# Kernel optimization log

Measured on AMD Instinct MI355X. Metric: run time of the kernel, lower is better.

## Reference

```python
import jax, jax.numpy as jnp
import numpy as np

B, D_IN, HID, LAT, K = 8192, 1024, 2048, 256, 4096

def setup_inputs() -> dict:
    key = jax.random.key(0)
    ks = jax.random.split(key, 16)
    s = lambda fan_in: 1.0 / np.sqrt(fan_in)
    inp = {
        'x':  jax.random.normal(ks[0], (B, D_IN), jnp.float32),
        # encoder MLP
        'W1': jax.random.normal(ks[1], (D_IN, HID), jnp.float32) * s(D_IN),
        'b1': jnp.zeros((HID,), jnp.float32),
        'W2': jax.random.normal(ks[2], (HID, HID), jnp.float32) * s(HID),
        'b2': jnp.zeros((HID,), jnp.float32),
        'W3': jax.random.normal(ks[3], (HID, LAT), jnp.float32) * s(HID),
        'b3': jnp.zeros((LAT,), jnp.float32),
        # codebook, uniform(-1/K, 1/K) per nn.init.uniform_
        'embed': jax.random.uniform(ks[4], (K, LAT), jnp.float32, -1.0 / K, 1.0 / K),
        # decoder MLP
        'D1': jax.random.normal(ks[5], (LAT, HID), jnp.float32) * s(LAT),
        'd1': jnp.zeros((HID,), jnp.float32),
        'D2': jax.random.normal(ks[6], (HID, HID), jnp.float32) * s(HID),
        'd2': jnp.zeros((HID,), jnp.float32),
        'D3': jax.random.normal(ks[7], (HID, D_IN), jnp.float32) * s(HID),
        'd3': jnp.zeros((D_IN,), jnp.float32),
    }
    return inp

def gelu(x):
    return jax.nn.gelu(x, approximate=False)  # torch nn.GELU default is exact erf

def reference(x, W1, b1, W2, b2, W3, b3, embed, D1, d1, D2, d2, D3, d3):
    sg = jax.lax.stop_gradient
    # encoder: [B, D_in] -> [B, latent]
    h = gelu(x @ W1 + b1)
    h = gelu(h @ W2 + b2)
    z_e = h @ W3 + b3
    # squared distances to codebook: ||z||^2 + ||e||^2 - 2 z.e -> [B, K]
    z_sq = jnp.sum(z_e * z_e, axis=1, keepdims=True)
    e_sq = jnp.sum(embed * embed, axis=1)[None, :]
    dist = z_sq + e_sq - 2.0 * (z_e @ embed.T)
    indices = jnp.argmin(dist, axis=1)            # [B]
    z_q = embed[indices]                          # [B, latent]
    commitment = jnp.mean((z_e - sg(z_q)) ** 2)
    codebook = jnp.mean((z_q - sg(z_e)) ** 2)
    vq_loss = codebook + 0.25 * commitment
    # straight-through estimator
    z_st = z_e + sg(z_q - z_e)
    # decoder: [B, latent] -> [B, D_in]
    g = gelu(z_st @ D1 + d1)
    g = gelu(g @ D2 + d2)
    x_recon = g @ D3 + d3
    return x_recon, vq_loss, indices
```

## Files before the change

kernel.cpp:

```cpp
#include <hip/hip_runtime.h>
#include <math.h>

#define B_    8192
#define DIN_  1024
#define HID_  2048
#define LAT_  256
#define KC_   4096

using bfrag8 = __attribute__((ext_vector_type(8))) short;
using short8 = __attribute__((ext_vector_type(8))) short;
using half8  = __attribute__((ext_vector_type(8))) _Float16;
using facc4  = __attribute__((ext_vector_type(4))) float;

__device__ __forceinline__ unsigned short f2bf(float f) {
    union { float f; unsigned int u; } c; c.f = f;
    unsigned int u = c.u;
    return (unsigned short)((u + 0x7FFFu + ((u >> 16) & 1u)) >> 16);
}

__device__ __forceinline__ unsigned short f2h_bits(float f) {
    union { _Float16 h; unsigned short u; } c; c.h = (_Float16)f;
    return c.u;
}

__device__ __forceinline__ void gload16(const unsigned short* g, unsigned short* l) {
    __builtin_amdgcn_global_load_lds(
        (const __attribute__((address_space(1))) void*)(g),
        (__attribute__((address_space(3))) void*)(l), 16, 0, 0);
}

template <int GELU, int OUT_SPLIT>
__global__ __launch_bounds__(512, 4) void gemm_split_f16_w8(
    const unsigned short* __restrict__ Ahi, const unsigned short* __restrict__ Alo,
    const unsigned short* __restrict__ WThi, const unsigned short* __restrict__ WTlo,
    const float* __restrict__ bias,
    unsigned short* __restrict__ Chi, unsigned short* __restrict__ Clo,
    float* __restrict__ Cf32,
    int M, int N, int K)
{
    __shared__ __align__(16) unsigned short AsH[128 * 64];
    __shared__ __align__(16) unsigned short AsL[128 * 64];
    __shared__ __align__(16) unsigned short WsH[128 * 64];
    __shared__ __align__(16) unsigned short WsL[128 * 64];

    const int tid  = threadIdx.x;
    const int wave = tid >> 6;
    const int lane = tid & 63;
    const int wm   = wave & 1;
    const int wn   = wave >> 1;
    const int quad = lane >> 4;
    const int ln   = lane & 15;
    const int n0 = blockIdx.x * 128;
    const int m0 = blockIdx.y * 128;

    const facc4 fz4 = {0.0f, 0.0f, 0.0f, 0.0f};
    facc4 accA[4][2] = {};
    facc4 accB[4][2] = {};
    facc4 master[4][2] = {};

    for (int k0 = 0; k0 < K; k0 += 64) {
#pragma unroll
        for (int i = 0; i < 2; ++i) {
            const int idx = i * 512 + tid;
            const int row = idx >> 3;
            const int gs  = (idx & 7) ^ (row & 7);
            const int wb  = i * 512 + (tid & 448);
            const size_t src = (size_t)(m0 + row) * K + k0 + gs * 8;
            gload16(&Ahi[src], &AsH[wb * 8]);
            gload16(&Alo[src], &AsL[wb * 8]);
        }
#pragma unroll
        for (int i = 0; i < 2; ++i) {
            const int idx = i * 512 + tid;
            const int row = idx >> 3;
            const int gs  = (idx & 7) ^ (row & 7);
            const int wb  = i * 512 + (tid & 448);
            const size_t src = (size_t)(n0 + row) * K + k0 + gs * 8;
            gload16(&WThi[src], &WsH[wb * 8]);
            gload16(&WTlo[src], &WsL[wb * 8]);
        }
        __syncthreads();
#pragma unroll
        for (int ks = 0; ks < 64; ks += 32) {
            const int gq = (ks >> 3) + quad;
            half8 aH[4], aL[4], bH[2], bL[2];
#pragma unroll
            for (int f = 0; f < 4; ++f) {
                const int row = wm * 64 + f * 16 + ln;
                const int off = row * 64 + ((gq ^ (ln & 7)) << 3);
                aH[f] = *reinterpret_cast<const half8*>(&AsH[off]);
                aL[f] = *reinterpret_cast<const half8*>(&AsL[off]);
            }
#pragma unroll
            for (int f = 0; f < 2; ++f) {
                const int row = wn * 32 + f * 16 + ln;
                const int off = row * 64 + ((gq ^ (ln & 7)) << 3);
                bH[f] = *reinterpret_cast<const half8*>(&WsH[off]);
                bL[f] = *reinterpret_cast<const half8*>(&WsL[off]);
            }
#pragma unroll
            for (int fm = 0; fm < 4; ++fm)
#pragma unroll
                for (int fn = 0; fn < 2; ++fn)
                    accA[fm][fn] = __builtin_amdgcn_mfma_f32_16x16x32_f16(
                        aH[fm], bH[fn], accA[fm][fn], 0, 0, 0);
#pragma unroll
            for (int fm = 0; fm < 4; ++fm)
#pragma unroll
                for (int fn = 0; fn < 2; ++fn)
                    accB[fm][fn] = __builtin_amdgcn_mfma_f32_16x16x32_f16(
                        aH[fm], bL[fn], accB[fm][fn], 0, 0, 0);
#pragma unroll
            for (int fm = 0; fm < 4; ++fm)
#pragma unroll
                for (int fn = 0; fn < 2; ++fn)
                    accB[fm][fn] = __builtin_amdgcn_mfma_f32_16x16x32_f16(
                        aL[fm], bH[fn], accB[fm][fn], 0, 0, 0);
        }
        __syncthreads();
        if ((k0 & 192) == 192) {
#pragma unroll
            for (int fm = 0; fm < 4; ++fm)
#pragma unroll
                for (int fn = 0; fn < 2; ++fn) {
                    master[fm][fn] += accA[fm][fn];
                    accA[fm][fn] = fz4;
                }
        }
    }

    const double SC_HI = 0.015625;
    const double SC_LO = 3.814697265625e-06;
#pragma unroll
    for (int fn = 0; fn < 2; ++fn) {
        const int col = n0 + wn * 32 + fn * 16 + ln;
        const double bb = (double)bias[col];
#pragma unroll
        for (int fm = 0; fm < 4; ++fm) {
            const int rbase = m0 + wm * 64 + fm * 16 + quad * 4;
#pragma unroll
            for (int r = 0; r < 4; ++r) {
                double v = (double)master[fm][fn][r] * SC_HI
                         + (double)accB[fm][fn][r] * SC_LO + bb;
                if (GELU) v = 0.5 * v * (1.0 + erf(v * 0.70710678118654752440));
                const float hf = (float)v;
                if (OUT_SPLIT == 1 || OUT_SPLIT == 2) {
                    const _Float16 hi = (_Float16)hf;
                    const float lo = (hf - (float)hi) * 4096.0f;
                    union { _Float16 h; unsigned short u; } c1, c2;
                    c1.h = hi; c2.h = (_Float16)lo;
                    Chi[(size_t)(rbase + r) * N + col] = c1.u;
                    Clo[(size_t)(rbase + r) * N + col] = c2.u;
                }
                if (OUT_SPLIT == 0 || OUT_SPLIT == 2) {
                    Cf32[(size_t)(rbase + r) * N + col] = hf;
                }
            }
        }
    }
}

template <int GELU, int OUT_SPLIT>
__global__ __launch_bounds__(256, 3) void gemm_split_f16(
    const unsigned short* __restrict__ Ahi, const unsigned short* __restrict__ Alo,
    const unsigned short* __restrict__ WThi, const unsigned short* __restrict__ WTlo,
    const float* __restrict__ bias,
    unsigned short* __restrict__ Chi, unsigned short* __restrict__ Clo,
    float* __restrict__ Cf32,
    int M, int N, int K)
{
    __shared__ __align__(16) unsigned short AsH[128 * 64];
    __shared__ __align__(16) unsigned short AsL[128 * 64];
    __shared__ __align__(16) unsigned short WsH[64 * 64];
    __shared__ __align__(16) unsigned short WsL[64 * 64];

    const int tid  = threadIdx.x;
    const int wave = tid >> 6;
    const int lane = tid & 63;
    const int wm   = wave & 1;
    const int wn   = wave >> 1;
    const int quad = lane >> 4;
    const int ln   = lane & 15;
    const int n0 = blockIdx.x * 64;
    const int m0 = blockIdx.y * 128;

    const facc4 fz4 = {0.0f, 0.0f, 0.0f, 0.0f};
    facc4 accA[4][2] = {};
    facc4 accB[4][2] = {};
    facc4 master[4][2] = {};

    for (int k0 = 0; k0 < K; k0 += 64) {
#pragma unroll
        for (int i = 0; i < 4; ++i) {
            const int idx = i * 256 + tid;
            const int row = idx >> 3;
            const int gs  = (idx & 7) ^ (row & 7);
            const int wb  = i * 256 + (tid & 192);
            const size_t src = (size_t)(m0 + row) * K + k0 + gs * 8;
            gload16(&Ahi[src], &AsH[wb * 8]);
            gload16(&Alo[src], &AsL[wb * 8]);
        }
#pragma unroll
        for (int i = 0; i < 2; ++i) {
            const int idx = i * 256 + tid;
            const int row = idx >> 3;
            const int gs  = (idx & 7) ^ (row & 7);
            const int wb  = i * 256 + (tid & 192);
            const size_t src = (size_t)(n0 + row) * K + k0 + gs * 8;
            gload16(&WThi[src], &WsH[wb * 8]);
            gload16(&WTlo[src], &WsL[wb * 8]);
        }
        __syncthreads();
#pragma unroll
        for (int ks = 0; ks < 64; ks += 32) {
            const int gq = (ks >> 3) + quad;
            half8 aH[4], aL[4], bH[2], bL[2];
#pragma unroll
            for (int f = 0; f < 4; ++f) {
                const int row = wm * 64 + f * 16 + ln;
                const int off = row * 64 + ((gq ^ (ln & 7)) << 3);
                aH[f] = *reinterpret_cast<const half8*>(&AsH[off]);
                aL[f] = *reinterpret_cast<const half8*>(&AsL[off]);
            }
#pragma unroll
            for (int f = 0; f < 2; ++f) {
                const int row = wn * 32 + f * 16 + ln;
                const int off = row * 64 + ((gq ^ (ln & 7)) << 3);
                bH[f] = *reinterpret_cast<const half8*>(&WsH[off]);
                bL[f] = *reinterpret_cast<const half8*>(&WsL[off]);
            }
#pragma unroll
            for (int fm = 0; fm < 4; ++fm)
#pragma unroll
                for (int fn = 0; fn < 2; ++fn)
                    accA[fm][fn] = __builtin_amdgcn_mfma_f32_16x16x32_f16(
                        aH[fm], bH[fn], accA[fm][fn], 0, 0, 0);
#pragma unroll
            for (int fm = 0; fm < 4; ++fm)
#pragma unroll
                for (int fn = 0; fn < 2; ++fn)
                    accB[fm][fn] = __builtin_amdgcn_mfma_f32_16x16x32_f16(
                        aH[fm], bL[fn], accB[fm][fn], 0, 0, 0);
#pragma unroll
            for (int fm = 0; fm < 4; ++fm)
#pragma unroll
                for (int fn = 0; fn < 2; ++fn)
                    accB[fm][fn] = __builtin_amdgcn_mfma_f32_16x16x32_f16(
                        aL[fm], bH[fn], accB[fm][fn], 0, 0, 0);
        }
        __syncthreads();
        if ((k0 & 192) == 192) {
#pragma unroll
            for (int fm = 0; fm < 4; ++fm)
#pragma unroll
                for (int fn = 0; fn < 2; ++fn) {
                    master[fm][fn] += accA[fm][fn];
                    accA[fm][fn] = fz4;
                }
        }
    }

    const double SC_HI = 0.015625;
    const double SC_LO = 3.814697265625e-06;
#pragma unroll
    for (int fn = 0; fn < 2; ++fn) {
        const int col = n0 + wn * 32 + fn * 16 + ln;
        const double bb = (double)bias[col];
#pragma unroll
        for (int fm = 0; fm < 4; ++fm) {
            const int rbase = m0 + wm * 64 + fm * 16 + quad * 4;
#pragma unroll
            for (int r = 0; r < 4; ++r) {
                double v = (double)master[fm][fn][r] * SC_HI
                         + (double)accB[fm][fn][r] * SC_LO + bb;
                if (GELU) v = 0.5 * v * (1.0 + erf(v * 0.70710678118654752440));
                const float hf = (float)v;
                if (OUT_SPLIT == 1 || OUT_SPLIT == 2) {
                    const _Float16 hi = (_Float16)hf;
                    const float lo = (hf - (float)hi) * 4096.0f;
                    union { _Float16 h; unsigned short u; } c1, c2;
                    c1.h = hi; c2.h = (_Float16)lo;
                    Chi[(size_t)(rbase + r) * N + col] = c1.u;
                    Clo[(size_t)(rbase + r) * N + col] = c2.u;
                }
                if (OUT_SPLIT == 0 || OUT_SPLIT == 2) {
                    Cf32[(size_t)(rbase + r) * N + col] = hf;
                }
            }
        }
    }
}

__global__ __launch_bounds__(256) void split_scaled_f16x2(
    const float* __restrict__ X, unsigned short* __restrict__ Xhi,
    unsigned short* __restrict__ Xlo, int n4, float scale)
{
    const int i = blockIdx.x * 256 + threadIdx.x;
    if (i >= n4) return;
    const float4 v = reinterpret_cast<const float4*>(X)[i];
    ushort4 h, l;
    {
        const float s = v.x * scale;
        _Float16 a = (_Float16)s; h.x = f2h_bits((float)a); l.x = f2h_bits((s - (float)a) * 4096.0f);
    }
    {
        const float s = v.y * scale;
        _Float16 a = (_Float16)s; h.y = f2h_bits((float)a); l.y = f2h_bits((s - (float)a) * 4096.0f);
    }
    {
        const float s = v.z * scale;
        _Float16 a = (_Float16)s; h.z = f2h_bits((float)a); l.z = f2h_bits((s - (float)a) * 4096.0f);
    }
    {
        const float s = v.w * scale;
        _Float16 a = (_Float16)s; h.w = f2h_bits((float)a); l.w = f2h_bits((s - (float)a) * 4096.0f);
    }
    reinterpret_cast<ushort4*>(Xhi)[i] = h;
    reinterpret_cast<ushort4*>(Xlo)[i] = l;
}

__global__ __launch_bounds__(64) void emb_prep(
    const float* __restrict__ E, float* __restrict__ esq,
    unsigned short* __restrict__ Ehi, unsigned short* __restrict__ Elo,
    float* __restrict__ loss_slot)
{
    const int r = blockIdx.x;
    const float4 v = reinterpret_cast<const float4*>(E + (size_t)r * LAT_)[threadIdx.x];
    ushort4 h, l;
    {
        const float s = v.x * 65536.0f;
        _Float16 a = (_Float16)s; h.x = f2h_bits((float)a); l.x = f2h_bits((s - (float)a) * 4096.0f);
    }
    {
        const float s = v.y * 65536.0f;
        _Float16 a = (_Float16)s; h.y = f2h_bits((float)a); l.y = f2h_bits((s - (float)a) * 4096.0f);
    }
    {
        const float s = v.z * 65536.0f;
        _Float16 a = (_Float16)s; h.z = f2h_bits((float)a); l.z = f2h_bits((s - (float)a) * 4096.0f);
    }
    {
        const float s = v.w * 65536.0f;
        _Float16 a = (_Float16)s; h.w = f2h_bits((float)a); l.w = f2h_bits((s - (float)a) * 4096.0f);
    }
    reinterpret_cast<ushort4*>(Ehi + (size_t)r * LAT_)[threadIdx.x] = h;
    reinterpret_cast<ushort4*>(Elo + (size_t)r * LAT_)[threadIdx.x] = l;
    double s = (double)v.x * v.x + (double)v.y * v.y + (double)v.z * v.z + (double)v.w * v.w;
#pragma unroll
    for (int off = 32; off; off >>= 1) s += __shfl_down(s, off, 64);
    if (threadIdx.x == 0) {
        esq[r] = (float)s;
        if (r == 0) *loss_slot = 0.0f;
    }
}

__global__ __launch_bounds__(256) void wsplit_transpose(
    const float* __restrict__ W, unsigned short* __restrict__ WThi,
    unsigned short* __restrict__ WTlo, int K, int N)
{
    __shared__ float t[32][33];
    const int k0 = blockIdx.x * 32;
    const int n0 = blockIdx.y * 32;
    const int x = threadIdx.x;
    const int y = threadIdx.y;
#pragma unroll
    for (int i = 0; i < 4; ++i)
        t[y + i * 8][x] = W[(size_t)(k0 + y + i * 8) * N + n0 + x];
    __syncthreads();
#pragma unroll
    for (int i = 0; i < 4; ++i) {
        const float w = t[x][y + i * 8] * 64.0f;
        const _Float16 hi = (_Float16)w;
        const float lo = (w - (float)hi) * 4096.0f;
        WThi[(size_t)(n0 + y + i * 8) * K + k0 + x] = f2h_bits((float)hi);
        WTlo[(size_t)(n0 + y + i * 8) * K + k0 + x] = f2h_bits(lo);
    }
}

__global__ __launch_bounds__(256, 2) void vq_argmin_mfma(
    const unsigned short* __restrict__ Zhi, const unsigned short* __restrict__ Zlo,
    const unsigned short* __restrict__ Ehi, const unsigned short* __restrict__ Elo,
    const float* __restrict__ esq, const float* __restrict__ zsq,
    float* __restrict__ pval, int* __restrict__ pidx)
{
    __shared__ __align__(16) unsigned short ZsH[128 * 64];
    __shared__ __align__(16) unsigned short ZsL[128 * 64];
    __shared__ __align__(16) unsigned short EsH[64 * 64];
    __shared__ __align__(16) unsigned short EsL[64 * 64];
    __shared__ float rbv[128][2];
    __shared__ int   rbi[128][2];

    const int tid  = threadIdx.x;
    const int wave = tid >> 6;
    const int lane = tid & 63;
    const int wm   = wave & 1;
    const int wn   = wave >> 1;
    const int quad = lane >> 4;
    const int ln   = lane & 15;
    const int m0    = blockIdx.x * 128;
    const int split = blockIdx.y;

    float zsqv[4][4];
#pragma unroll
    for (int fm = 0; fm < 4; ++fm) {
        const float4 q = *reinterpret_cast<const float4*>(
            &zsq[m0 + wm * 64 + fm * 16 + quad * 4]);
        zsqv[fm][0] = q.x; zsqv[fm][1] = q.y; zsqv[fm][2] = q.z; zsqv[fm][3] = q.w;
    }

    float bestv[4][4];
    int   besti[4][4];
#pragma unroll
    for (int a = 0; a < 4; ++a)
#pragma unroll
        for (int b = 0; b < 4; ++b) { bestv[a][b] = 3.4e38f; besti[a][b] = 0; }

    for (int nt = 0; nt < 8; ++nt) {
        const int n0 = split * 512 + nt * 64;
        facc4 accA[4][2] = {};
        facc4 accB[4][2] = {};
        for (int k0 = 0; k0 < 256; k0 += 64) {
            __syncthreads();
#pragma unroll
            for (int i = 0; i < 4; ++i) {
                const int idx = i * 256 + tid;
                const int row = idx >> 3;
                const int gs  = (idx & 7) ^ (row & 7);
                const int wb  = i * 256 + (tid & 192);
                const size_t src = (size_t)(m0 + row) * LAT_ + k0 + gs * 8;
                gload16(&Zhi[src], &ZsH[wb * 8]);
                gload16(&Zlo[src], &ZsL[wb * 8]);
            }
#pragma unroll
            for (int i = 0; i < 2; ++i) {
                const int idx = i * 256 + tid;
                const int row = idx >> 3;
                const int gs  = (idx & 7) ^ (row & 7);
                const int wb  = i * 256 + (tid & 192);
                const size_t src = (size_t)(n0 + row) * LAT_ + k0 + gs * 8;
                gload16(&Ehi[src], &EsH[wb * 8]);
                gload16(&Elo[src], &EsL[wb * 8]);
            }
            __syncthreads();
#pragma unroll
            for (int ks = 0; ks < 64; ks += 32) {
                const int gq = (ks >> 3) + quad;
                half8 aH[4], aL[4], bH[2], bL[2];
#pragma unroll
                for (int f = 0; f < 4; ++f) {
                    const int row = wm * 64 + f * 16 + ln;
                    const int off = row * 64 + ((gq ^ (ln & 7)) << 3);
                    aH[f] = *reinterpret_cast<const half8*>(&ZsH[off]);
                    aL[f] = *reinterpret_cast<const half8*>(&ZsL[off]);
                }
#pragma unroll
                for (int f = 0; f < 2; ++f) {
                    const int row = wn * 32 + f * 16 + ln;
                    const int off = row * 64 + ((gq ^ (ln & 7)) << 3);
                    bH[f] = *reinterpret_cast<const half8*>(&EsH[off]);
                    bL[f] = *reinterpret_cast<const half8*>(&EsL[off]);
                }
#pragma unroll
                for (int fm = 0; fm < 4; ++fm)
#pragma unroll
                    for (int fn = 0; fn < 2; ++fn)
                        accA[fm][fn] = __builtin_amdgcn_mfma_f32_16x16x32_f16(
                            aH[fm], bH[fn], accA[fm][fn], 0, 0, 0);
#pragma unroll
                for (int fm = 0; fm < 4; ++fm)
#pragma unroll
                    for (int fn = 0; fn < 2; ++fn)
                        accB[fm][fn] = __builtin_amdgcn_mfma_f32_16x16x32_f16(
                            aH[fm], bL[fn], accB[fm][fn], 0, 0, 0);
#pragma unroll
                for (int fm = 0; fm < 4; ++fm)
#pragma unroll
                    for (int fn = 0; fn < 2; ++fn)
                        accB[fm][fn] = __builtin_amdgcn_mfma_f32_16x16x32_f16(
                            aL[fm], bH[fn], accB[fm][fn], 0, 0, 0);
            }
        }
#pragma unroll
        for (int fm = 0; fm < 4; ++fm)
#pragma unroll
            for (int fn = 0; fn < 2; ++fn) {
                const int n = n0 + wn * 32 + fn * 16 + ln;
                const float es = esq[n];
#pragma unroll
                for (int r = 0; r < 4; ++r) {
                    const float pa = accA[fm][fn][r] * 0x1p-15f;
                    const float pb = accB[fm][fn][r] * 0x1p-27f;
                    const float t2m = pa + pb;
                    const float sc = (zsqv[fm][r] + es) - t2m;
                    if (sc < bestv[fm][r]) { bestv[fm][r] = sc; besti[fm][r] = n; }
                }
            }
    }

#pragma unroll
    for (int fm = 0; fm < 4; ++fm)
#pragma unroll
        for (int r = 0; r < 4; ++r) {
            float v0 = bestv[fm][r]; int i0 = besti[fm][r];
#pragma unroll
            for (int mask = 1; mask < 16; mask <<= 1) {
                const float v2 = __shfl_xor(v0, mask, 64);
                const int   i2 = __shfl_xor(i0, mask, 64);
                if (v2 < v0 || (v2 == v0 && i2 < i0)) { v0 = v2; i0 = i2; }
            }
            bestv[fm][r] = v0; besti[fm][r] = i0;
        }

    if (ln == 0) {
#pragma unroll
        for (int fm = 0; fm < 4; ++fm)
#pragma unroll
            for (int r = 0; r < 4; ++r) {
                const int rl = wm * 64 + fm * 16 + quad * 4 + r;
                rbv[rl][wn] = bestv[fm][r];
                rbi[rl][wn] = besti[fm][r];
            }
    }
    __syncthreads();
    if (tid < 128) {
        float bv = rbv[tid][0]; int bi = rbi[tid][0];
        const float v = rbv[tid][1]; const int ix = rbi[tid][1];
        if (v < bv || (v == bv && ix < bi)) { bv = v; bi = ix; }
        pval[(size_t)(m0 + tid) * 8 + split] = bv;
        pidx[(m0 + tid) * 8 + split] = bi;
    }
}

template <int OUT_BF16>
__global__ __launch_bounds__(256) void gemm_mfma_bf16(
    const unsigned short* __restrict__ A,
    const unsigned short* __restrict__ WT,
    const float* __restrict__ bias,
    void* __restrict__ Cout,
    int M, int N, int K)
{
    __shared__ __align__(16) unsigned short As[128 * 64];
    __shared__ __align__(16) unsigned short Bs[128 * 64];

    const int tid  = threadIdx.x;
    const int wave = tid >> 6;
    const int lane = tid & 63;
    const int wm   = wave & 1;
    const int wn   = wave >> 1;
    const int quad = lane >> 4;
    const int ln   = lane & 15;
    const int m0 = blockIdx.x * 128;
    const int n0 = blockIdx.y * 128;

    facc4 acc[4][4] = {};

    for (int k0 = 0; k0 < K; k0 += 64) {
#pragma unroll
        for (int i = 0; i < 4; ++i) {
            const int idx = i * 256 + tid;
            const int row = idx >> 3;
            const int c8  = (idx & 7) * 8;
            const int wb  = i * 256 + (tid & 192);
            gload16(&A[(size_t)(m0 + row) * K + k0 + c8], &As[wb * 8]);
            gload16(&WT[(size_t)(n0 + row) * K + k0 + c8], &Bs[wb * 8]);
        }
        __syncthreads();
#pragma unroll
        for (int ks = 0; ks < 64; ks += 32) {
            bfrag8 am[4], bn[4];
#pragma unroll
            for (int f = 0; f < 4; ++f) {
                am[f] = *reinterpret_cast<const bfrag8*>(
                    &As[(wm * 64 + f * 16 + ln) * 64 + ks + quad * 8]);
                bn[f] = *reinterpret_cast<const bfrag8*>(
                    &Bs[(wn * 64 + f * 16 + ln) * 64 + ks + quad * 8]);
            }
#pragma unroll
            for (int fm = 0; fm < 4; ++fm)
#pragma unroll
                for (int fn = 0; fn < 4; ++fn)
                    acc[fm][fn] = __builtin_amdgcn_mfma_f32_16x16x32_bf16(
                        am[fm], bn[fn], acc[fm][fn], 0, 0, 0);
        }
        __syncthreads();
    }

#pragma unroll
    for (int fn = 0; fn < 4; ++fn) {
        const int col = n0 + wn * 64 + fn * 16 + ln;
        const float bf = bias[col];
#pragma unroll
        for (int fm = 0; fm < 4; ++fm) {
            const int rbase = m0 + wm * 64 + fm * 16 + quad * 4;
#pragma unroll
            for (int r = 0; r < 4; ++r) {
                float v = acc[fm][fn][r] + bf;
                if (OUT_BF16) {
                    v = 0.5f * v * (1.0f + erff(v * 0.70710678118654752440f));
                    ((unsigned short*)Cout)[(size_t)(rbase + r) * N + col] = f2bf(v);
                } else {
                    ((float*)Cout)[(size_t)(rbase + r) * N + col] = v;
                }
            }
        }
    }
}

__global__ __launch_bounds__(256) void cast_transpose_w3(
    const float* __restrict__ D1w, unsigned short* __restrict__ wt1,
    const float* __restrict__ D2w, unsigned short* __restrict__ wt2,
    const float* __restrict__ D3w, unsigned short* __restrict__ wt3)
{
    const int bid = blockIdx.x;
    const float* W; unsigned short* WT; int K, N, kt, nt;
    if (bid < 512)        { W = D1w; WT = wt1; K = LAT_; N = HID_; kt = bid & 7;  nt = bid >> 3; }
    else if (bid < 4608)  { const int l = bid - 512;  W = D2w; WT = wt2; K = HID_; N = HID_; kt = l & 63; nt = l >> 6; }
    else                  { const int l = bid - 4608; W = D3w; WT = wt3; K = HID_; N = DIN_; kt = l & 63; nt = l >> 6; }

    __shared__ float t[32][33];
    const int k0 = kt * 32;
    const int n0 = nt * 32;
    const int x = threadIdx.x;
    const int y = threadIdx.y;
#pragma unroll
    for (int i = 0; i < 4; ++i)
        t[y + i * 8][x] = W[(size_t)(k0 + y + i * 8) * N + n0 + x];
    __syncthreads();
#pragma unroll
    for (int i = 0; i < 4; ++i)
        WT[(size_t)(n0 + y + i * 8) * K + k0 + x] = f2bf(t[x][y + i * 8]);
}

__global__ __launch_bounds__(64) void rowsq_kernel(
    const float* __restrict__ X, float* __restrict__ out,
    float* __restrict__ loss_slot)
{
    const int r = blockIdx.x;
    const float4 v = reinterpret_cast<const float4*>(X + (size_t)r * LAT_)[threadIdx.x];
    double s = (double)v.x * v.x + (double)v.y * v.y + (double)v.z * v.z + (double)v.w * v.w;
#pragma unroll
    for (int off = 32; off; off >>= 1) s += __shfl_down(s, off, 64);
    if (threadIdx.x == 0) {
        out[r] = (float)s;
        if (loss_slot != nullptr && r == 0) *loss_slot = 0.0f;
    }
}

__global__ __launch_bounds__(64) void vq_finalize(
    const float* __restrict__ pval, const int* __restrict__ pidx,
    const float* __restrict__ Z, const float* __restrict__ E,
    unsigned short* __restrict__ zqb, float* __restrict__ out_idx,
    float* __restrict__ loss_slot)
{
    const int row = blockIdx.x;
    __shared__ int sidx;
    if (threadIdx.x == 0) {
        float bv = pval[row * 8]; int bi = pidx[row * 8];
#pragma unroll
        for (int s = 1; s < 8; ++s) {
            const float v = pval[row * 8 + s]; const int ix = pidx[row * 8 + s];
            if (v < bv || (v == bv && ix < bi)) { bv = v; bi = ix; }
        }
        sidx = bi;
        out_idx[row] = (float)bi;
    }
    __syncthreads();
    const int idx = sidx;
    const float4 e = reinterpret_cast<const float4*>(E + (size_t)idx * LAT_)[threadIdx.x];
    const float4 z = reinterpret_cast<const float4*>(Z + (size_t)row * LAT_)[threadIdx.x];
    ushort4 q; q.x = f2bf(e.x); q.y = f2bf(e.y); q.z = f2bf(e.z); q.w = f2bf(e.w);
    reinterpret_cast<ushort4*>(zqb + (size_t)row * LAT_)[threadIdx.x] = q;
    const float dx = z.x - e.x, dy = z.y - e.y, dz = z.z - e.z, dw = z.w - e.w;
    float s = dx * dx + dy * dy + dz * dz + dw * dw;
#pragma unroll
    for (int off = 32; off; off >>= 1) s += __shfl_down(s, off, 64);
    if (threadIdx.x == 0)
        atomicAdd(loss_slot, s * (1.25f / ((float)B_ * (float)LAT_)));
}

extern "C" void kernel_launch(void* const* d_in, const int* in_sizes, int n_in,
                              void* d_out, int out_size, void* d_ws, size_t ws_size,
                              hipStream_t stream)
{
    const float* x   = (const float*)d_in[0];
    const float* W1  = (const float*)d_in[1];
    const float* b1  = (const float*)d_in[2];
    const float* W2  = (const float*)d_in[3];
    const float* b2  = (const float*)d_in[4];
    const float* W3  = (const float*)d_in[5];
    const float* b3  = (const float*)d_in[6];
    const float* emb = (const float*)d_in[7];
    const float* D1  = (const float*)d_in[8];
    const float* d1  = (const float*)d_in[9];
    const float* D2  = (const float*)d_in[10];
    const float* d2  = (const float*)d_in[11];
    const float* D3  = (const float*)d_in[12];
    const float* d3  = (const float*)d_in[13];
    float* out = (float*)d_out;

    char* ws = (char*)d_ws;
    const size_t MB = 1u << 20;
    unsigned short* h1hi = (unsigned short*)(ws);
    unsigned short* h1lo = (unsigned short*)(ws + 32 * MB);
    unsigned short* zehi = (unsigned short*)(ws);
    unsigned short* zelo = (unsigned short*)(ws + 4 * MB);
    unsigned short* g1b  = (unsigned short*)(ws);
    unsigned short* zqb  = (unsigned short*)(ws + 32 * MB);
    unsigned short* g2b  = (unsigned short*)(ws + 32 * MB);
    unsigned short* xhi  = (unsigned short*)(ws + 64 * MB);
    unsigned short* xlo  = (unsigned short*)(ws + 80 * MB);
    unsigned short* h2hi = (unsigned short*)(ws + 64 * MB);
    unsigned short* h2lo = (unsigned short*)(ws + 96 * MB);
    unsigned short* wt1  = (unsigned short*)(ws + 64 * MB);
    unsigned short* wt2  = (unsigned short*)(ws + 65 * MB);
    unsigned short* wt3  = (unsigned short*)(ws + 73 * MB);
    float* ze = (float*)(ws + 128 * MB);
    unsigned short* w1thi = (unsigned short*)(ws + 136 * MB);
    unsigned short* w1tlo = (unsigned short*)(ws + 140 * MB);
    unsigned short* w2thi = (unsigned short*)(ws + 136 * MB);
    unsigned short* w2tlo = (unsigned short*)(ws + 144 * MB);
    unsigned short* w3thi = (unsigned short*)(ws + 136 * MB);
    unsigned short* w3tlo = (unsigned short*)(ws + 137 * MB);
    unsigned short* ehi   = (unsigned short*)(ws + 144 * MB);
    unsigned short* elo   = (unsigned short*)(ws + 146 * MB);
    float* esq  = (float*)(ws + 152 * MB);
    float* zsq  = (float*)(ws + 152 * MB + 64 * 1024);
    float* pval = (float*)(ws + 152 * MB + 128 * 1024);
    int*   pidx = (int*)  (ws + 152 * MB + 384 * 1024);

    float* loss_slot = out + (size_t)B_ * DIN_;
    float* out_idx   = loss_slot + 1;

    split_scaled_f16x2<<<(B_ * DIN_ / 4 + 255) / 256, 256, 0, stream>>>(
        x, xhi, xlo, B_ * DIN_ / 4, 1.0f);
    wsplit_transpose<<<dim3(DIN_ / 32, HID_ / 32), dim3(32, 8), 0, stream>>>(W1, w1thi, w1tlo, DIN_, HID_);

    gemm_split_f16_w8<1, 1><<<dim3(HID_ / 128, B_ / 128), 512, 0, stream>>>(
        xhi, xlo, w1thi, w1tlo, b1, h1hi, h1lo, nullptr, B_, HID_, DIN_);

    wsplit_transpose<<<dim3(HID_ / 32, HID_ / 32), dim3(32, 8), 0, stream>>>(W2, w2thi, w2tlo, HID_, HID_);

    gemm_split_f16_w8<1, 1><<<dim3(HID_ / 128, B_ / 128), 512, 0, stream>>>(
        h1hi, h1lo, w2thi, w2tlo, b2, h2hi, h2lo, nullptr, B_, HID_, HID_);

    emb_prep<<<KC_, 64, 0, stream>>>(emb, esq, ehi, elo, loss_slot);
    wsplit_transpose<<<dim3(HID_ / 32, LAT_ / 32), dim3(32, 8), 0, stream>>>(W3, w3thi, w3tlo, HID_, LAT_);

    gemm_split_f16<0, 2><<<dim3(LAT_ / 64, B_ / 128), 256, 0, stream>>>(
        h2hi, h2lo, w3thi, w3tlo, b3, zehi, zelo, ze, B_, LAT_, HID_);

    rowsq_kernel<<<B_, 64, 0, stream>>>(ze, zsq, nullptr);

    cast_transpose_w3<<<6656, dim3(32, 8), 0, stream>>>(D1, wt1, D2, wt2, D3, wt3);

    vq_argmin_mfma<<<dim3(B_ / 128, 8), 256, 0, stream>>>(
        zehi, zelo, ehi, elo, esq, zsq, pval, pidx);
    vq_finalize<<<B_, 64, 0, stream>>>(pval, pidx, ze, emb, zqb, out_idx, loss_slot);

    gemm_mfma_bf16<1><<<dim3(B_ / 128, HID_ / 128), 256, 0, stream>>>(zqb, wt1, d1, (void*)g1b, B_, HID_, LAT_);
    gemm_mfma_bf16<1><<<dim3(B_ / 128, HID_ / 128), 256, 0, stream>>>(g1b, wt2, d2, (void*)g2b, B_, HID_, HID_);
    gemm_mfma_bf16<0><<<dim3(B_ / 128, DIN_ / 128), 256, 0, stream>>>(g2b, wt3, d3, (void*)out, B_, DIN_, HID_);
}
```

Baseline: 1.134 ms.

## Fuse prep kernels into two launches and retile split-f16 GEMMs

Merges the x split, W1/W2/W3 split-transposes into one prep_all launch, and the embedding prep plus decoder weight cast-transposes into one mid_prep launch, rearranging workspace so the buffers don't alias. The encoder GEMMs drop the 512-thread 128x128 tile for the 256-thread 128x64 kernel, and the W3 GEMM moves to a new 64x64 tile kernel to produce more blocks for the narrow N=256 output. The aim is fewer launches and better occupancy and grid fill. The cost is smaller tiles with less operand reuse and extra workspace footprint from the new layout.

Result: no change. 1.154 ms (+1.8%).

```diff
diff --git a/kernel.cpp b/kernel.cpp
--- a/kernel.cpp
+++ b/kernel.cpp
@@ -30,7 +30,7 @@
 }
 
 template <int GELU, int OUT_SPLIT>
-__global__ __launch_bounds__(512, 4) void gemm_split_f16_w8(
+__global__ __launch_bounds__(256, 3) void gemm_split_f16(
     const unsigned short* __restrict__ Ahi, const unsigned short* __restrict__ Alo,
     const unsigned short* __restrict__ WThi, const unsigned short* __restrict__ WTlo,
     const float* __restrict__ bias,
@@ -40,8 +40,8 @@
 {
     __shared__ __align__(16) unsigned short AsH[128 * 64];
     __shared__ __align__(16) unsigned short AsL[128 * 64];
-    __shared__ __align__(16) unsigned short WsH[128 * 64];
-    __shared__ __align__(16) unsigned short WsL[128 * 64];
+    __shared__ __align__(16) unsigned short WsH[64 * 64];
+    __shared__ __align__(16) unsigned short WsL[64 * 64];
 
     const int tid  = threadIdx.x;
     const int wave = tid >> 6;
@@ -50,7 +50,7 @@
     const int wn   = wave >> 1;
     const int quad = lane >> 4;
     const int ln   = lane & 15;
-    const int n0 = blockIdx.x * 128;
+    const int n0 = blockIdx.x * 64;
     const int m0 = blockIdx.y * 128;
 
     const facc4 fz4 = {0.0f, 0.0f, 0.0f, 0.0f};
@@ -60,21 +60,21 @@
 
     for (int k0 = 0; k0 < K; k0 += 64) {
 #pragma unroll
-        for (int i = 0; i < 2; ++i) {
-            const int idx = i * 512 + tid;
+        for (int i = 0; i < 4; ++i) {
+            const int idx = i * 256 + tid;
             const int row = idx >> 3;
             const int gs  = (idx & 7) ^ (row & 7);
-            const int wb  = i * 512 + (tid & 448);
+            const int wb  = i * 256 + (tid & 192);
             const size_t src = (size_t)(m0 + row) * K + k0 + gs * 8;
             gload16(&Ahi[src], &AsH[wb * 8]);
             gload16(&Alo[src], &AsL[wb * 8]);
         }
 #pragma unroll
         for (int i = 0; i < 2; ++i) {
-            const int idx = i * 512 + tid;
+            const int idx = i * 256 + tid;
             const int row = idx >> 3;
             const int gs  = (idx & 7) ^ (row & 7);
-            const int wb  = i * 512 + (tid & 448);
+            const int wb  = i * 256 + (tid & 192);
             const size_t src = (size_t)(n0 + row) * K + k0 + gs * 8;
             gload16(&WThi[src], &WsH[wb * 8]);
             gload16(&WTlo[src], &WsL[wb * 8]);
@@ -161,7 +161,7 @@
 }
 
 template <int GELU, int OUT_SPLIT>
-__global__ __launch_bounds__(256, 3) void gemm_split_f16(
+__global__ __launch_bounds__(256, 4) void gemm_split_f16_m64(
     const unsigned short* __restrict__ Ahi, const unsigned short* __restrict__ Alo,
     const unsigned short* __restrict__ WThi, const unsigned short* __restrict__ WTlo,
     const float* __restrict__ bias,
@@ -169,8 +169,8 @@
     float* __restrict__ Cf32,
     int M, int N, int K)
 {
-    __shared__ __align__(16) unsigned short AsH[128 * 64];
-    __shared__ __align__(16) unsigned short AsL[128 * 64];
+    __shared__ __align__(16) unsigned short AsH[64 * 64];
+    __shared__ __align__(16) unsigned short AsL[64 * 64];
     __shared__ __align__(16) unsigned short WsH[64 * 64];
     __shared__ __align__(16) unsigned short WsL[64 * 64];
 
@@ -182,16 +182,16 @@
     const int quad = lane >> 4;
     const int ln   = lane & 15;
     const int n0 = blockIdx.x * 64;
-    const int m0 = blockIdx.y * 128;
+    const int m0 = blockIdx.y * 64;
 
     const facc4 fz4 = {0.0f, 0.0f, 0.0f, 0.0f};
-    facc4 accA[4][2] = {};
-    facc4 accB[4][2] = {};
-    facc4 master[4][2] = {};
+    facc4 accA[2][2] = {};
+    facc4 accB[2][2] = {};
+    facc4 master[2][2] = {};
 
     for (int k0 = 0; k0 < K; k0 += 64) {
 #pragma unroll
-        for (int i = 0; i < 4; ++i) {
+        for (int i = 0; i < 2; ++i) {
             const int idx = i * 256 + tid;
             const int row = idx >> 3;
             const int gs  = (idx & 7) ^ (row & 7);
@@ -214,10 +214,10 @@
 #pragma unroll
         for (int ks = 0; ks < 64; ks += 32) {
             const int gq = (ks >> 3) + quad;
-            half8 aH[4], aL[4], bH[2], bL[2];
-#pragma unroll
-            for (int f = 0; f < 4; ++f) {
-                const int row = wm * 64 + f * 16 + ln;
+            half8 aH[2], aL[2], bH[2], bL[2];
+#pragma unroll
+            for (int f = 0; f < 2; ++f) {
+                const int row = wm * 32 + f * 16 + ln;
                 const int off = row * 64 + ((gq ^ (ln & 7)) << 3);
                 aH[f] = *reinterpret_cast<const half8*>(&AsH[off]);
                 aL[f] = *reinterpret_cast<const half8*>(&AsL[off]);
@@ -230,19 +230,19 @@
                 bL[f] = *reinterpret_cast<const half8*>(&WsL[off]);
             }
 #pragma unroll
-            for (int fm = 0; fm < 4; ++fm)
+            for (int fm = 0; fm < 2; ++fm)
 #pragma unroll
                 for (int fn = 0; fn < 2; ++fn)
                     accA[fm][fn] = __builtin_amdgcn_mfma_f32_16x16x32_f16(
                         aH[fm], bH[fn], accA[fm][fn], 0, 0, 0);
 #pragma unroll
-            for (int fm = 0; fm < 4; ++fm)
+            for (int fm = 0; fm < 2; ++fm)
 #pragma unroll
                 for (int fn = 0; fn < 2; ++fn)
                     accB[fm][fn] = __builtin_amdgcn_mfma_f32_16x16x32_f16(
                         aH[fm], bL[fn], accB[fm][fn], 0, 0, 0);
 #pragma unroll
-            for (int fm = 0; fm < 4; ++fm)
+            for (int fm = 0; fm < 2; ++fm)
 #pragma unroll
                 for (int fn = 0; fn < 2; ++fn)
                     accB[fm][fn] = __builtin_amdgcn_mfma_f32_16x16x32_f16(
@@ -251,7 +251,7 @@
         __syncthreads();
         if ((k0 & 192) == 192) {
 #pragma unroll
-            for (int fm = 0; fm < 4; ++fm)
+            for (int fm = 0; fm < 2; ++fm)
 #pragma unroll
                 for (int fn = 0; fn < 2; ++fn) {
                     master[fm][fn] += accA[fm][fn];
@@ -267,8 +267,8 @@
         const int col = n0 + wn * 32 + fn * 16 + ln;
         const double bb = (double)bias[col];
 #pragma unroll
-        for (int fm = 0; fm < 4; ++fm) {
-            const int rbase = m0 + wm * 64 + fm * 16 + quad * 4;
+        for (int fm = 0; fm < 2; ++fm) {
+            const int rbase = m0 + wm * 32 + fm * 16 + quad * 4;
 #pragma unroll
             for (int r = 0; r < 4; ++r) {
                 double v = (double)master[fm][fn][r] * SC_HI
@@ -291,78 +291,50 @@
     }
 }
 
-__global__ __launch_bounds__(256) void split_scaled_f16x2(
+__global__ __launch_bounds__(256) void prep_all(
     const float* __restrict__ X, unsigned short* __restrict__ Xhi,
-    unsigned short* __restrict__ Xlo, int n4, float scale)
-{
-    const int i = blockIdx.x * 256 + threadIdx.x;
-    if (i >= n4) return;
-    const float4 v = reinterpret_cast<const float4*>(X)[i];
-    ushort4 h, l;
-    {
-        const float s = v.x * scale;
-        _Float16 a = (_Float16)s; h.x = f2h_bits((float)a); l.x = f2h_bits((s - (float)a) * 4096.0f);
-    }
-    {
-        const float s = v.y * scale;
-        _Float16 a = (_Float16)s; h.y = f2h_bits((float)a); l.y = f2h_bits((s - (float)a) * 4096.0f);
-    }
-    {
-        const float s = v.z * scale;
-        _Float16 a = (_Float16)s; h.z = f2h_bits((float)a); l.z = f2h_bits((s - (float)a) * 4096.0f);
-    }
-    {
-        const float s = v.w * scale;
-        _Float16 a = (_Float16)s; h.w = f2h_bits((float)a); l.w = f2h_bits((s - (float)a) * 4096.0f);
-    }
-    reinterpret_cast<ushort4*>(Xhi)[i] = h;
-    reinterpret_cast<ushort4*>(Xlo)[i] = l;
-}
-
-__global__ __launch_bounds__(64) void emb_prep(
-    const float* __restrict__ E, float* __restrict__ esq,
-    unsigned short* __restrict__ Ehi, unsigned short* __restrict__ Elo,
-    float* __restrict__ loss_slot)
-{
-    const int r = blockIdx.x;
-    const float4 v = reinterpret_cast<const float4*>(E + (size_t)r * LAT_)[threadIdx.x];
-    ushort4 h, l;
-    {
-        const float s = v.x * 65536.0f;
-        _Float16 a = (_Float16)s; h.x = f2h_bits((float)a); l.x = f2h_bits((s - (float)a) * 4096.0f);
-    }
-    {
-        const float s = v.y * 65536.0f;
-        _Float16 a = (_Float16)s; h.y = f2h_bits((float)a); l.y = f2h_bits((s - (float)a) * 4096.0f);
-    }
-    {
-        const float s = v.z * 65536.0f;
-        _Float16 a = (_Float16)s; h.z = f2h_bits((float)a); l.z = f2h_bits((s - (float)a) * 4096.0f);
-    }
-    {
-        const float s = v.w * 65536.0f;
-        _Float16 a = (_Float16)s; h.w = f2h_bits((float)a); l.w = f2h_bits((s - (float)a) * 4096.0f);
-    }
-    reinterpret_cast<ushort4*>(Ehi + (size_t)r * LAT_)[threadIdx.x] = h;
-    reinterpret_cast<ushort4*>(Elo + (size_t)r * LAT_)[threadIdx.x] = l;
-    double s = (double)v.x * v.x + (double)v.y * v.y + (double)v.z * v.z + (double)v.w * v.w;
-#pragma unroll
-    for (int off = 32; off; off >>= 1) s += __shfl_down(s, off, 64);
-    if (threadIdx.x == 0) {
-        esq[r] = (float)s;
-        if (r == 0) *loss_slot = 0.0f;
-    }
-}
-
-__global__ __launch_bounds__(256) void wsplit_transpose(
-    const float* __restrict__ W, unsigned short* __restrict__ WThi,
-    unsigned short* __restrict__ WTlo, int K, int N)
-{
+    unsigned short* __restrict__ Xlo,
+    const float* __restrict__ W1w, unsigned short* __restrict__ w1thi,
+    unsigned short* __restrict__ w1tlo,
+    const float* __restrict__ W2w, unsigned short* __restrict__ w2thi,
+    unsigned short* __restrict__ w2tlo,
+    const float* __restrict__ W3w, unsigned short* __restrict__ w3thi,
+    unsigned short* __restrict__ w3tlo)
+{
+    const int bid = blockIdx.x;
+    const int tid = threadIdx.x;
+
+    if (bid < 8192) {
+        const int i = bid * 256 + tid;
+        const float4 v = reinterpret_cast<const float4*>(X)[i];
+        ushort4 h, l;
+        {
+            _Float16 a = (_Float16)v.x; h.x = f2h_bits((float)a); l.x = f2h_bits((v.x - (float)a) * 4096.0f);
+        }
+        {
+            _Float16 a = (_Float16)v.y; h.y = f2h_bits((float)a); l.y = f2h_bits((v.y - (float)a) * 4096.0f);
+        }
+        {
+            _Float16 a = (_Float16)v.z; h.z = f2h_bits((float)a); l.z = f2h_bits((v.z - (float)a) * 4096.0f);
+        }
+        {
+            _Float16 a = (_Float16)v.w; h.w = f2h_bits((float)a); l.w = f2h_bits((v.w - (float)a) * 4096.0f);
+        }
+        reinterpret_cast<ushort4*>(Xhi)[i] = h;
+        reinterpret_cast<ushort4*>(Xlo)[i] = l;
+        return;
+    }
+
+    const float* W; unsigned short* WThi; unsigned short* WTlo; int K, N, kt, nt;
+    if (bid < 10240)      { const int l = bid - 8192;  W = W1w; WThi = w1thi; WTlo = w1tlo; K = DIN_; N = HID_; kt = l & 31; nt = l >> 5; }
+    else if (bid < 14336) { const int l = bid - 10240; W = W2w; WThi = w2thi; WTlo = w2tlo; K = HID_; N = HID_; kt = l & 63; nt = l >> 6; }
+    else                  { const int l = bid - 14336; W = W3w; WThi = w3thi; WTlo = w3tlo; K = HID_; N = LAT_; kt = l & 63; nt = l >> 6; }
+
     __shared__ float t[32][33];
-    const int k0 = blockIdx.x * 32;
-    const int n0 = blockIdx.y * 32;
-    const int x = threadIdx.x;
-    const int y = threadIdx.y;
+    const int k0 = kt * 32;
+    const int n0 = nt * 32;
+    const int x = tid & 31;
+    const int y = tid >> 5;
 #pragma unroll
     for (int i = 0; i < 4; ++i)
         t[y + i * 8][x] = W[(size_t)(k0 + y + i * 8) * N + n0 + x];
@@ -375,6 +347,71 @@
         WThi[(size_t)(n0 + y + i * 8) * K + k0 + x] = f2h_bits((float)hi);
         WTlo[(size_t)(n0 + y + i * 8) * K + k0 + x] = f2h_bits(lo);
     }
+}
+
+__global__ __launch_bounds__(256) void mid_prep(
+    const float* __restrict__ E, float* __restrict__ esq,
+    unsigned short* __restrict__ Ehi, unsigned short* __restrict__ Elo,
+    float* __restrict__ loss_slot,
+    const float* __restrict__ D1w, unsigned short* __restrict__ wt1,
+    const float* __restrict__ D2w, unsigned short* __restrict__ wt2,
+    const float* __restrict__ D3w, unsigned short* __restrict__ wt3)
+{
+    const int bid = blockIdx.x;
+    const int tid = threadIdx.x;
+
+    if (bid < 1024) {
+        const int w    = tid >> 6;
+        const int lane = tid & 63;
+        const int r    = bid * 4 + w;
+        const float4 v = reinterpret_cast<const float4*>(E + (size_t)r * LAT_)[lane];
+        ushort4 h, l;
+        {
+            const float s = v.x * 65536.0f;
+            _Float16 a = (_Float16)s; h.x = f2h_bits((float)a); l.x = f2h_bits((s - (float)a) * 4096.0f);
+        }
+        {
+            const float s = v.y * 65536.0f;
+            _Float16 a = (_Float16)s; h.y = f2h_bits((float)a); l.y = f2h_bits((s - (float)a) * 4096.0f);
+        }
+        {
+            const float s = v.z * 65536.0f;
+            _Float16 a = (_Float16)s; h.z = f2h_bits((float)a); l.z = f2h_bits((s - (float)a) * 4096.0f);
+        }
+        {
+            const float s = v.w * 65536.0f;
+            _Float16 a = (_Float16)s; h.w = f2h_bits((float)a); l.w = f2h_bits((s - (float)a) * 4096.0f);
+        }
+        reinterpret_cast<ushort4*>(Ehi + (size_t)r * LAT_)[lane] = h;
+        reinterpret_cast<ushort4*>(Elo + (size_t)r * LAT_)[lane] = l;
+        double s = (double)v.x * v.x + (double)v.y * v.y + (double)v.z * v.z + (double)v.w * v.w;
+#pragma unroll
+        for (int off = 32; off; off >>= 1) s += __shfl_down(s, off, 64);
+        if (lane == 0) {
+            esq[r] = (float)s;
+            if (r == 0) *loss_slot = 0.0f;
+        }
+        return;
+    }
+
+    const int cb = bid - 1024;
+    const float* W; unsigned short* WT; int K, N, kt, nt;
+    if (cb < 512)        { W = D1w; WT = wt1; K = LAT_; N = HID_; kt = cb & 7;  nt = cb >> 3; }
+    else if (cb < 4608)  { const int l = cb - 512;  W = D2w; WT = wt2; K = HID_; N = HID_; kt = l & 63; nt = l >> 6; }
+    else                 { const int l = cb - 4608; W = D3w; WT = wt3; K = HID_; N = DIN_; kt = l & 63; nt = l >> 6; }
+
+    __shared__ float t[32][33];
+    const int k0 = kt * 32;
+    const int n0 = nt * 32;
+    const int x = tid & 31;
+    const int y = tid >> 5;
+#pragma unroll
+    for (int i = 0; i < 4; ++i)
+        t[y + i * 8][x] = W[(size_t)(k0 + y + i * 8) * N + n0 + x];
+    __syncthreads();
+#pragma unroll
+    for (int i = 0; i < 4; ++i)
+        WT[(size_t)(n0 + y + i * 8) * K + k0 + x] = f2bf(t[x][y + i * 8]);
 }
 
 __global__ __launch_bounds__(256, 2) void vq_argmin_mfma(
@@ -604,31 +641,6 @@
             }
         }
     }
-}
-
-__global__ __launch_bounds__(256) void cast_transpose_w3(
-    const float* __restrict__ D1w, unsigned short* __restrict__ wt1,
-    const float* __restrict__ D2w, unsigned short* __restrict__ wt2,
-    const float* __restrict__ D3w, unsigned short* __restrict__ wt3)
-{
-    const int bid = blockIdx.x;
-    const float* W; unsigned short* WT; int K, N, kt, nt;
-    if (bid < 512)        { W = D1w; WT = wt1; K = LAT_; N = HID_; kt = bid & 7;  nt = bid >> 3; }
-    else if (bid < 4608)  { const int l = bid - 512;  W = D2w; WT = wt2; K = HID_; N = HID_; kt = l & 63; nt = l >> 6; }
-    else                  { const int l = bid - 4608; W = D3w; WT = wt3; K = HID_; N = DIN_; kt = l & 63; nt = l >> 6; }
-
-    __shared__ float t[32][33];
-    const int k0 = kt * 32;
-    const int n0 = nt * 32;
-    const int x = threadIdx.x;
-    const int y = threadIdx.y;
-#pragma unroll
-    for (int i = 0; i < 4; ++i)
-        t[y + i * 8][x] = W[(size_t)(k0 + y + i * 8) * N + n0 + x];
-    __syncthreads();
-#pragma unroll
-    for (int i = 0; i < 4; ++i)
-        WT[(size_t)(n0 + y + i * 8) * K + k0 + x] = f2bf(t[x][y + i * 8]);
 }
 
 __global__ __launch_bounds__(64) void rowsq_kernel(
@@ -711,47 +723,42 @@
     unsigned short* xlo  = (unsigned short*)(ws + 80 * MB);
     unsigned short* h2hi = (unsigned short*)(ws + 64 * MB);
     unsigned short* h2lo = (unsigned short*)(ws + 96 * MB);
-    unsigned short* wt1  = (unsigned short*)(ws + 64 * MB);
-    unsigned short* wt2  = (unsigned short*)(ws + 65 * MB);
-    unsigned short* wt3  = (unsigned short*)(ws + 73 * MB);
+    unsigned short* w1thi = (unsigned short*)(ws + 96 * MB);
+    unsigned short* w1tlo = (unsigned short*)(ws + 100 * MB);
     float* ze = (float*)(ws + 128 * MB);
-    unsigned short* w1thi = (unsigned short*)(ws + 136 * MB);
-    unsigned short* w1tlo = (unsigned short*)(ws + 140 * MB);
     unsigned short* w2thi = (unsigned short*)(ws + 136 * MB);
     unsigned short* w2tlo = (unsigned short*)(ws + 144 * MB);
-    unsigned short* w3thi = (unsigned short*)(ws + 136 * MB);
-    unsigned short* w3tlo = (unsigned short*)(ws + 137 * MB);
+    unsigned short* wt2   = (unsigned short*)(ws + 136 * MB);
     unsigned short* ehi   = (unsigned short*)(ws + 144 * MB);
     unsigned short* elo   = (unsigned short*)(ws + 146 * MB);
-    float* esq  = (float*)(ws + 152 * MB);
-    float* zsq  = (float*)(ws + 152 * MB + 64 * 1024);
-    float* pval = (float*)(ws + 152 * MB + 128 * 1024);
-    int*   pidx = (int*)  (ws + 152 * MB + 384 * 1024);
+    unsigned short* wt3   = (unsigned short*)(ws + 148 * MB);
+    unsigned short* w3thi = (unsigned short*)(ws + 152 * MB);
+    unsigned short* w3tlo = (unsigned short*)(ws + 153 * MB);
+    float* esq  = (float*)(ws + 154 * MB);
+    float* zsq  = (float*)(ws + 154 * MB + 64 * 1024);
+    float* pval = (float*)(ws + 154 * MB + 128 * 1024);
+    int*   pidx = (int*)  (ws + 154 * MB + 384 * 1024);
+    unsigned short* wt1 = (unsigned short*)(ws + 155 * MB);
 
     float* loss_slot = out + (size_t)B_ * DIN_;
     float* out_idx   = loss_slot + 1;
 
-    split_scaled_f16x2<<<(B_ * DIN_ / 4 + 255) / 256, 256, 0, stream>>>(
-        x, xhi, xlo, B_ * DIN_ / 4, 1.0f);
-    wsplit_transpose<<<dim3(DIN_ / 32, HID_ / 32), dim3(32, 8), 0, stream>>>(W1, w1thi, w1tlo, DIN_, HID_);
-
-    gemm_split_f16_w8<1, 1><<<dim3(HID_ / 128, B_ / 128), 512, 0, stream>>>(
+    prep_all<<<14848, 256, 0, stream>>>(
+        x, xhi, xlo, W1, w1thi, w1tlo, W2, w2thi, w2tlo, W3, w3thi, w3tlo);
+
+    gemm_split_f16<1, 1><<<dim3(HID_ / 64, B_ / 128), 256, 0, stream>>>(
         xhi, xlo, w1thi, w1tlo, b1, h1hi, h1lo, nullptr, B_, HID_, DIN_);
 
-    wsplit_transpose<<<dim3(HID_ / 32, HID_ / 32), dim3(32, 8), 0, stream>>>(W2, w2thi, w2tlo, HID_, HID_);
-
-    gemm_split_f16_w8<1, 1><<<dim3(HID_ / 128, B_ / 128), 512, 0, stream>>>(
+    gemm_split_f16<1, 1><<<dim3(HID_ / 64, B_ / 128), 256, 0, stream>>>(
         h1hi, h1lo, w2thi, w2tlo, b2, h2hi, h2lo, nullptr, B_, HID_, HID_);
 
-    emb_prep<<<KC_, 64, 0, stream>>>(emb, esq, ehi, elo, loss_slot);
-    wsplit_transpose<<<dim3(HID_ / 32, LAT_ / 32), dim3(32, 8), 0, stream>>>(W3, w3thi, w3tlo, HID_, LAT_);
-
-    gemm_split_f16<0, 2><<<dim3(LAT_ / 64, B_ / 128), 256, 0, stream>>>(
+    mid_prep<<<7680, 256, 0, stream>>>(
+        emb, esq, ehi, elo, loss_slot, D1, wt1, D2, wt2, D3, wt3);
+
+    gemm_split_f16_m64<0, 2><<<dim3(LAT_ / 64, B_ / 64), 256, 0, stream>>>(
         h2hi, h2lo, w3thi, w3tlo, b3, zehi, zelo, ze, B_, LAT_, HID_);
 
     rowsq_kernel<<<B_, 64, 0, stream>>>(ze, zsq, nullptr);
-
-    cast_transpose_w3<<<6656, dim3(32, 8), 0, stream>>>(D1, wt1, D2, wt2, D3, wt3);
 
     vq_argmin_mfma<<<dim3(B_ / 128, 8), 256, 0, stream>>>(
         zehi, zelo, ehi, elo, esq, zsq, pval, pidx);
```
